# Optimization experiments

Hardware: AMD Instinct MI355X
Metric: run time of the kernel (lower is better)

## Reference

```python
import jax, jax.numpy as jnp
import numpy as np

N, E = 30000, 600000
D_NODE, E_DIM, H1, H2, D_OUT = 128, 128, 256, 128, 128


def setup_inputs() -> dict:
    key = jax.random.key(0)
    ks = jax.random.split(key, 24)
    w = lambda k, shape: jax.random.normal(k, shape, jnp.float32) * 0.05
    return {
        "node_feat": jax.random.normal(ks[0], (N, D_NODE), jnp.float32),
        "src": jax.random.randint(ks[1], (E,), 0, N, jnp.int32),
        "dst": jax.random.randint(ks[2], (E,), 0, N, jnp.int32),
        "W_e1": w(ks[3], (2 * D_NODE + E_DIM, H1)), "b_e1": w(ks[4], (H1,)),
        "W_e2": w(ks[5], (H1, E_DIM)), "b_e2": w(ks[6], (E_DIM,)),
        "W_n1": w(ks[7], (D_NODE + E_DIM, H1)), "b_n1": w(ks[8], (H1,)),
        "W_n2": w(ks[9], (H1, H2)), "b_n2": w(ks[10], (H2,)),
        "W_el1": w(ks[11], (2 * H2, H1)), "b_el1": w(ks[12], (H1,)),
        "W_el2": w(ks[13], (H1, E_DIM)), "b_el2": w(ks[14], (E_DIM,)),
        "W_logit": w(ks[15], (E_DIM, 2)), "b_logit": w(ks[16], (2,)),
        "W_nro": w(ks[17], (H2, D_OUT)), "b_nro": w(ks[18], (D_OUT,)),
        "W_ero": w(ks[19], (E_DIM, D_OUT)), "b_ero": w(ks[20], (D_OUT,)),
        "msg_passing_steps": 2,
    }


def reference(node_feat, src, dst,
              W_e1, b_e1, W_e2, b_e2,
              W_n1, b_n1, W_n2, b_n2,
              W_el1, b_el1, W_el2, b_el2,
              W_logit, b_logit, W_nro, b_nro, W_ero, b_ero,
              msg_passing_steps):
    n_nodes = node_feat.shape[0]
    edge_dim = W_e2.shape[1]
    # incoming messages 'h', initialized to zeros
    h = jnp.zeros((n_nodes, edge_dim), node_feat.dtype)
    for _ in range(msg_passing_steps):
        # apply_edges: edge_feat = fc_edge2(relu(fc_edge([h_src, nf_src, nf_dst])))
        inp = jnp.concatenate([h[src], node_feat[src], node_feat[dst]], axis=-1)  # [E, edge_dim+2*D]
        edge_feat = jax.nn.relu(inp @ W_e1 + b_e1) @ W_e2 + b_e2                   # [E, edge_dim]
        # update_all with fn.sum: scatter-sum messages into destination nodes
        h = jax.ops.segment_sum(edge_feat, dst, num_segments=n_nodes)
    # apply_nodes: node_feat <- fc_node2(relu(fc_node([node_feat, h])))
    nf = jax.nn.relu(jnp.concatenate([node_feat, h], axis=-1) @ W_n1 + b_n1) @ W_n2 + b_n2  # [N, H2]
    n_out = nf @ W_nro + b_nro
    # compute_edge_logits: symmetric edge MLP over updated node reps
    s, d = nf[src], nf[dst]
    edge_mlp = lambda x: jax.nn.relu(x @ W_el1 + b_el1) @ W_el2 + b_el2
    comb = edge_mlp(jnp.concatenate([s, d], axis=-1)) + edge_mlp(jnp.concatenate([d, s], axis=-1))
    e_out_readout = comb @ W_ero + b_ero
    e_out = comb @ W_logit + b_logit
    return n_out, e_out_readout, e_out
```

## Files before the change

kernel.cpp:

```cpp
#include <hip/hip_runtime.h>
#include <hip/hip_bf16.h>

typedef __bf16 bf16;
typedef unsigned short u16;
typedef bf16 bf16x8 __attribute__((ext_vector_type(8)));
typedef bf16 bf16x4 __attribute__((ext_vector_type(4)));
typedef float f32x4 __attribute__((ext_vector_type(4)));

constexpr int NN = 30000;
constexpr int NE = 600000;
constexpr int D  = 128;

__device__ inline f32x4 mfma16(bf16x8 a, bf16x8 b, f32x4 c) {
    return __builtin_amdgcn_mfma_f32_16x16x32_bf16(a, b, c, 0, 0, 0);
}
__device__ inline bf16x8 ld8(const bf16* p) {
    return *reinterpret_cast<const bf16x8*>(p);
}
__device__ inline bf16x8 cvt8(const float* p) {
    float4 v0 = reinterpret_cast<const float4*>(p)[0];
    float4 v1 = reinterpret_cast<const float4*>(p)[1];
    bf16x8 r;
    r[0] = (bf16)v0.x; r[1] = (bf16)v0.y; r[2] = (bf16)v0.z; r[3] = (bf16)v0.w;
    r[4] = (bf16)v1.x; r[5] = (bf16)v1.y; r[6] = (bf16)v1.z; r[7] = (bf16)v1.w;
    return r;
}
__device__ inline int swz512(int row, int byteInRow) {
    return row * 512 + (byteInRow ^ ((row & 15) << 4));
}

struct TMat { const float* src; bf16* dst; int K; int Nc; };
struct TPack { TMat m[12]; };

__global__ void transpose_cast_kernel(TPack p) {
    TMat mm = p.m[blockIdx.x];
    int total = mm.K * mm.Nc;
    for (int idx = blockIdx.y * blockDim.x + threadIdx.x; idx < total;
         idx += gridDim.y * blockDim.x) {
        int c = idx / mm.K;
        int k = idx - c * mm.K;
        mm.dst[idx] = (bf16)mm.src[k * mm.Nc + c];
    }
}

__global__ void fuse_kernel(const float* __restrict__ W_el2,
                            const float* __restrict__ W_ero,
                            const float* __restrict__ W_logit,
                            const float* __restrict__ b_el2,
                            const float* __restrict__ b_ero,
                            const float* __restrict__ b_logit,
                            bf16* __restrict__ W2eroT, bf16* __restrict__ W2lgT,
                            float* __restrict__ b2ero, float* __restrict__ b2lg) {
    int k = blockIdx.x;
    int c = threadIdx.x;
    if (c >= 144) return;
    if (k < 256) {
        if (c < 128) {
            float s = 0.f;
            for (int j = 0; j < 128; ++j) s += W_el2[k * 128 + j] * W_ero[j * 128 + c];
            W2eroT[c * 256 + k] = (bf16)s;
        } else {
            int cc = c - 128;
            float s = 0.f;
            if (cc < 2) for (int j = 0; j < 128; ++j) s += W_el2[k * 128 + j] * W_logit[j * 2 + cc];
            W2lgT[cc * 256 + k] = (bf16)s;
        }
    } else {
        if (c < 128) {
            float s = b_ero[c];
            for (int j = 0; j < 128; ++j) s += 2.f * b_el2[j] * W_ero[j * 128 + c];
            b2ero[c] = s;
        } else if (c < 130) {
            int cc = c - 128;
            float s = b_logit[cc];
            for (int j = 0; j < 128; ++j) s += 2.f * b_el2[j] * W_logit[j * 2 + cc];
            b2lg[cc] = s;
        }
    }
}

__global__ void fuse2_kernel(const float* __restrict__ W_e2,
                             const float* __restrict__ W_e1,
                             const float* __restrict__ W_n1,
                             const float* __restrict__ b_e2,
                             bf16* __restrict__ WcsT, bf16* __restrict__ WcnT,
                             float* __restrict__ bcs, float* __restrict__ bcn) {
    int k = blockIdx.x;
    int c = threadIdx.x;
    if (k < 256) {
        float s1 = 0.f, s2 = 0.f;
        for (int j = 0; j < 128; ++j) {
            float w = W_e2[k * 128 + j];
            s1 += w * W_e1[j * 256 + c];
            s2 += w * W_n1[(128 + j) * 256 + c];
        }
        WcsT[c * 256 + k] = (bf16)s1;
        WcnT[c * 256 + k] = (bf16)s2;
    } else {
        float s1 = 0.f, s2 = 0.f;
        for (int j = 0; j < 128; ++j) {
            float b = b_e2[j];
            s1 += b * W_e1[j * 256 + c];
            s2 += b * W_n1[(128 + j) * 256 + c];
        }
        bcs[c] = s1;
        bcn[c] = s2;
    }
}

__global__ void hist_kernel(const int* __restrict__ dst, int* __restrict__ counts) {
    int e = blockIdx.x * blockDim.x + threadIdx.x;
    if (e < NE) atomicAdd(counts + dst[e], 1);
}

__global__ void scan_kernel(const int* __restrict__ counts, int* __restrict__ offsets,
                            int* __restrict__ cursor) {
    __shared__ int part[1024];
    const int t = threadIdx.x;
    const int base = t * 30;
    int local[30];
    int s = 0;
#pragma unroll
    for (int i = 0; i < 30; ++i) {
        int idx = base + i;
        int v = (idx < NN) ? counts[idx] : 0;
        local[i] = s;
        s += v;
    }
    part[t] = s;
    __syncthreads();
    for (int off = 1; off < 1024; off <<= 1) {
        int x = (t >= off) ? part[t - off] : 0;
        __syncthreads();
        part[t] += x;
        __syncthreads();
    }
    int chunkExcl = (t == 0) ? 0 : part[t - 1];
#pragma unroll
    for (int i = 0; i < 30; ++i) {
        int idx = base + i;
        if (idx < NN) {
            int excl = chunkExcl + local[i];
            offsets[idx] = excl;
            cursor[idx] = excl;
        }
    }
    if (t == 0) offsets[NN] = NE;
}

__global__ void scatter_kernel(const int* __restrict__ src, const int* __restrict__ dst,
                               int* __restrict__ cursor, int* __restrict__ perm,
                               u16* __restrict__ srcS, u16* __restrict__ dstS) {
    int e = blockIdx.x * blockDim.x + threadIdx.x;
    if (e < NE) {
        int d = dst[e];
        int p = atomicAdd(cursor + d, 1);
        perm[p] = e;
        srcS[p] = (u16)src[e];
        dstS[p] = (u16)d;
    }
}

template<bool IN_BF16>
__global__ void __launch_bounds__(256, 4)
node_pre_kernel(const float* __restrict__ inF, const bf16* __restrict__ inB,
                const bf16* __restrict__ WT,
                const float* __restrict__ bias0,
                bf16* __restrict__ O1, bf16* __restrict__ O2) {
    const int half = blockIdx.y;
    const int r0 = blockIdx.x * 64;
    const int t = threadIdx.x, wv = t >> 6, l = t & 63, lr = l & 15, qk = l >> 4;
    int row[4];
#pragma unroll
    for (int m = 0; m < 4; ++m) { int r = r0 + m * 16 + lr; row[m] = r < NN ? r : NN - 1; }
    int coln[4];
#pragma unroll
    for (int n = 0; n < 4; ++n) coln[n] = wv * 64 + n * 16 + lr;
    f32x4 acc[4][4];
#pragma unroll
    for (int m = 0; m < 4; ++m)
#pragma unroll
        for (int n = 0; n < 4; ++n) acc[m][n] = 0.f;
#pragma unroll
    for (int ks = 0; ks < 4; ++ks) {
        const int kg = ks * 32 + qk * 8;
        bf16x8 a[4], b[4];
#pragma unroll
        for (int m = 0; m < 4; ++m)
            a[m] = IN_BF16 ? ld8(inB + row[m] * D + kg) : cvt8(inF + row[m] * D + kg);
#pragma unroll
        for (int n = 0; n < 4; ++n) b[n] = ld8(WT + (half * 256 + coln[n]) * 128 + kg);
#pragma unroll
        for (int m = 0; m < 4; ++m)
#pragma unroll
            for (int n = 0; n < 4; ++n) acc[m][n] = mfma16(a[m], b[n], acc[m][n]);
    }
    bf16* O = half ? O2 : O1;
#pragma unroll
    for (int n = 0; n < 4; ++n) {
        float bia = (half == 0 && bias0) ? bias0[coln[n]] : 0.f;
#pragma unroll
        for (int m = 0; m < 4; ++m)
#pragma unroll
            for (int j = 0; j < 4; ++j) {
                int gr = r0 + m * 16 + qk * 4 + j;
                if (gr < NN) O[gr * 256 + coln[n]] = (bf16)(acc[m][n][j] + bia);
            }
    }
}

__global__ void __launch_bounds__(256, 4)
s2_fused_kernel(const bf16* __restrict__ T, const bf16* __restrict__ WcsT,
                const float* __restrict__ bcs, const int* __restrict__ deg,
                bf16* __restrict__ S) {
    const int r0 = blockIdx.x * 64;
    const int t = threadIdx.x, wv = t >> 6, l = t & 63, lr = l & 15, qk = l >> 4;
    int row[4];
#pragma unroll
    for (int m = 0; m < 4; ++m) { int r = r0 + m * 16 + lr; row[m] = r < NN ? r : NN - 1; }
    int coln[4];
#pragma unroll
    for (int n = 0; n < 4; ++n) coln[n] = wv * 64 + n * 16 + lr;
    f32x4 acc[4][4];
#pragma unroll
    for (int m = 0; m < 4; ++m)
#pragma unroll
        for (int n = 0; n < 4; ++n) acc[m][n] = 0.f;
#pragma unroll
    for (int ks = 0; ks < 8; ++ks) {
        const int kg = ks * 32 + qk * 8;
        bf16x8 a[4], b[4];
#pragma unroll
        for (int m = 0; m < 4; ++m) a[m] = ld8(T + (size_t)row[m] * 256 + kg);
#pragma unroll
        for (int n = 0; n < 4; ++n) b[n] = ld8(WcsT + coln[n] * 256 + kg);
#pragma unroll
        for (int m = 0; m < 4; ++m)
#pragma unroll
            for (int n = 0; n < 4; ++n) acc[m][n] = mfma16(a[m], b[n], acc[m][n]);
    }
#pragma unroll
    for (int n = 0; n < 4; ++n) {
        float bw = bcs[coln[n]];
#pragma unroll
        for (int m = 0; m < 4; ++m)
#pragma unroll
            for (int j = 0; j < 4; ++j) {
                int gr = r0 + m * 16 + qk * 4 + j;
                if (gr < NN) {
                    int idx = gr * 256 + coln[n];
                    S[idx] = (bf16)((float)S[idx] + acc[m][n][j] + (float)deg[gr] * bw);
                }
            }
    }
}

__global__ void __launch_bounds__(256, 4)
s2_update_kernel(const float* __restrict__ h1, const bf16* __restrict__ WtopT,
                 bf16* __restrict__ S) {
    const int r0 = blockIdx.x * 64;
    const int t = threadIdx.x, wv = t >> 6, l = t & 63, lr = l & 15, qk = l >> 4;
    int row[4];
#pragma unroll
    for (int m = 0; m < 4; ++m) { int r = r0 + m * 16 + lr; row[m] = r < NN ? r : NN - 1; }
    int coln[4];
#pragma unroll
    for (int n = 0; n < 4; ++n) coln[n] = wv * 64 + n * 16 + lr;
    f32x4 acc[4][4];
#pragma unroll
    for (int m = 0; m < 4; ++m)
#pragma unroll
        for (int n = 0; n < 4; ++n) acc[m][n] = 0.f;
#pragma unroll
    for (int ks = 0; ks < 4; ++ks) {
        const int kg = ks * 32 + qk * 8;
        bf16x8 a[4], b[4];
#pragma unroll
        for (int m = 0; m < 4; ++m) a[m] = cvt8(h1 + (size_t)row[m] * D + kg);
#pragma unroll
        for (int n = 0; n < 4; ++n) b[n] = ld8(WtopT + coln[n] * 128 + kg);
#pragma unroll
        for (int m = 0; m < 4; ++m)
#pragma unroll
            for (int n = 0; n < 4; ++n) acc[m][n] = mfma16(a[m], b[n], acc[m][n]);
    }
#pragma unroll
    for (int n = 0; n < 4; ++n)
#pragma unroll
        for (int m = 0; m < 4; ++m)
#pragma unroll
            for (int j = 0; j < 4; ++j) {
                int gr = r0 + m * 16 + qk * 4 + j;
                if (gr < NN) {
                    int idx = gr * 256 + coln[n];
                    S[idx] = (bf16)((float)S[idx] + acc[m][n][j]);
                }
            }
}

__global__ void __launch_bounds__(256, 8)
seg_sum_kernel(const bf16* __restrict__ S, const bf16* __restrict__ Bm,
               const int* __restrict__ offsets, const u16* __restrict__ srcS,
               bf16* __restrict__ T) {
    const int gw = (blockIdx.x * blockDim.x + threadIdx.x) >> 6;
    if (gw >= NN) return;
    const int l = threadIdx.x & 63;
    const int beg = offsets[gw], end = offsets[gw + 1];
    bf16x4 bv = *reinterpret_cast<const bf16x4*>(Bm + (size_t)gw * 256 + l * 4);
    const float b0 = (float)bv[0], b1 = (float)bv[1], b2 = (float)bv[2], b3 = (float)bv[3];
    float t0 = 0.f, t1 = 0.f, t2 = 0.f, t3 = 0.f;
    int i = beg;
    for (; i + 4 <= end; i += 4) {
        int s0 = srcS[i], s1 = srcS[i + 1], s2 = srcS[i + 2], s3 = srcS[i + 3];
        bf16x4 a0 = *reinterpret_cast<const bf16x4*>(S + (size_t)s0 * 256 + l * 4);
        bf16x4 a1 = *reinterpret_cast<const bf16x4*>(S + (size_t)s1 * 256 + l * 4);
        bf16x4 a2 = *reinterpret_cast<const bf16x4*>(S + (size_t)s2 * 256 + l * 4);
        bf16x4 a3 = *reinterpret_cast<const bf16x4*>(S + (size_t)s3 * 256 + l * 4);
        float v;
        v = (float)a0[0] + b0; t0 += v > 0.f ? v : 0.f;
        v = (float)a0[1] + b1; t1 += v > 0.f ? v : 0.f;
        v = (float)a0[2] + b2; t2 += v > 0.f ? v : 0.f;
        v = (float)a0[3] + b3; t3 += v > 0.f ? v : 0.f;
        v = (float)a1[0] + b0; t0 += v > 0.f ? v : 0.f;
        v = (float)a1[1] + b1; t1 += v > 0.f ? v : 0.f;
        v = (float)a1[2] + b2; t2 += v > 0.f ? v : 0.f;
        v = (float)a1[3] + b3; t3 += v > 0.f ? v : 0.f;
        v = (float)a2[0] + b0; t0 += v > 0.f ? v : 0.f;
        v = (float)a2[1] + b1; t1 += v > 0.f ? v : 0.f;
        v = (float)a2[2] + b2; t2 += v > 0.f ? v : 0.f;
        v = (float)a2[3] + b3; t3 += v > 0.f ? v : 0.f;
        v = (float)a3[0] + b0; t0 += v > 0.f ? v : 0.f;
        v = (float)a3[1] + b1; t1 += v > 0.f ? v : 0.f;
        v = (float)a3[2] + b2; t2 += v > 0.f ? v : 0.f;
        v = (float)a3[3] + b3; t3 += v > 0.f ? v : 0.f;
    }
    for (; i < end; ++i) {
        int s0 = srcS[i];
        bf16x4 a0 = *reinterpret_cast<const bf16x4*>(S + (size_t)s0 * 256 + l * 4);
        float v;
        v = (float)a0[0] + b0; t0 += v > 0.f ? v : 0.f;
        v = (float)a0[1] + b1; t1 += v > 0.f ? v : 0.f;
        v = (float)a0[2] + b2; t2 += v > 0.f ? v : 0.f;
        v = (float)a0[3] + b3; t3 += v > 0.f ? v : 0.f;
    }
    bf16x4 o;
    o[0] = (bf16)t0; o[1] = (bf16)t1; o[2] = (bf16)t2; o[3] = (bf16)t3;
    *reinterpret_cast<bf16x4*>(T + (size_t)gw * 256 + l * 4) = o;
}

__global__ void __launch_bounds__(256, 2)
node_mlp_fused(const float* __restrict__ node_feat,
               const bf16* __restrict__ T2,
               const bf16* __restrict__ Wn1T,
               const bf16* __restrict__ WcnT,
               const bf16* __restrict__ Wn2T,
               const float* __restrict__ b_n1,
               const float* __restrict__ bcn,
               const int* __restrict__ deg,
               const float* __restrict__ b_n2,
               bf16* __restrict__ nf2_bf) {
    __shared__ __align__(16) char sH[64 * 512];
    const int t = threadIdx.x, wv = t >> 6, l = t & 63, lr = l & 15, qk = l >> 4;
    const int r0 = blockIdx.x * 64;
    int row[4];
#pragma unroll
    for (int m = 0; m < 4; ++m) { int r = r0 + m * 16 + lr; row[m] = r < NN ? r : NN - 1; }
    int coln[4];
#pragma unroll
    for (int n = 0; n < 4; ++n) coln[n] = wv * 64 + n * 16 + lr;
    f32x4 acc[4][4];
#pragma unroll
    for (int m = 0; m < 4; ++m)
#pragma unroll
        for (int n = 0; n < 4; ++n) acc[m][n] = 0.f;
#pragma unroll
    for (int ks = 0; ks < 4; ++ks) {
        const int kg = ks * 32 + qk * 8;
        bf16x8 a[4], b[4];
#pragma unroll
        for (int m = 0; m < 4; ++m) a[m] = cvt8(node_feat + (size_t)row[m] * D + kg);
#pragma unroll
        for (int n = 0; n < 4; ++n) b[n] = ld8(Wn1T + coln[n] * 256 + kg);
#pragma unroll
        for (int m = 0; m < 4; ++m)
#pragma unroll
            for (int n = 0; n < 4; ++n) acc[m][n] = mfma16(a[m], b[n], acc[m][n]);
    }
#pragma unroll
    for (int ks = 0; ks < 8; ++ks) {
        const int kg = ks * 32 + qk * 8;
        bf16x8 a[4], b[4];
#pragma unroll
        for (int m = 0; m < 4; ++m) a[m] = ld8(T2 + (size_t)row[m] * 256 + kg);
#pragma unroll
        for (int n = 0; n < 4; ++n) b[n] = ld8(WcnT + coln[n] * 256 + kg);
#pragma unroll
        for (int m = 0; m < 4; ++m)
#pragma unroll
            for (int n = 0; n < 4; ++n) acc[m][n] = mfma16(a[m], b[n], acc[m][n]);
    }
#pragma unroll
    for (int n = 0; n < 4; ++n) {
        float bia = b_n1[coln[n]];
        float bw  = bcn[coln[n]];
#pragma unroll
        for (int m = 0; m < 4; ++m)
#pragma unroll
            for (int j = 0; j < 4; ++j) {
                int r = m * 16 + qk * 4 + j;
                int gr = r0 + r;
                float dg = (gr < NN) ? (float)deg[gr] : 0.f;
                float v = acc[m][n][j] + bia + dg * bw;
                v = v > 0.f ? v : 0.f;
                *reinterpret_cast<bf16*>(sH + swz512(r, coln[n] * 2)) = (bf16)v;
            }
    }
    __syncthreads();
    int col2[2];
#pragma unroll
    for (int n = 0; n < 2; ++n) col2[n] = wv * 32 + n * 16 + lr;
    f32x4 acc2[4][2];
#pragma unroll
    for (int m = 0; m < 4; ++m)
#pragma unroll
        for (int n = 0; n < 2; ++n) acc2[m][n] = 0.f;
#pragma unroll
    for (int ks = 0; ks < 8; ++ks) {
        const int k0 = ks * 32 + qk * 8;
        bf16x8 a[4], b[2];
#pragma unroll
        for (int m = 0; m < 4; ++m)
            a[m] = *reinterpret_cast<const bf16x8*>(sH + swz512(m * 16 + lr, k0 * 2));
#pragma unroll
        for (int n = 0; n < 2; ++n) b[n] = ld8(Wn2T + col2[n] * 256 + k0);
#pragma unroll
        for (int m = 0; m < 4; ++m)
#pragma unroll
            for (int n = 0; n < 2; ++n) acc2[m][n] = mfma16(a[m], b[n], acc2[m][n]);
    }
#pragma unroll
    for (int n = 0; n < 2; ++n) {
        float bia = b_n2[col2[n]];
#pragma unroll
        for (int m = 0; m < 4; ++m)
#pragma unroll
            for (int j = 0; j < 4; ++j) {
                int gr = r0 + m * 16 + qk * 4 + j;
                if (gr < NN) nf2_bf[(size_t)gr * D + col2[n]] = (bf16)(acc2[m][n][j] + bia);
            }
    }
}

__global__ void __launch_bounds__(256, 2)
node_mlp_kernel(const float* __restrict__ node_feat,
                const float* __restrict__ h2,
                const bf16* __restrict__ Wn1T,
                const bf16* __restrict__ Wn2T,
                const float* __restrict__ b_n1,
                const float* __restrict__ b_n2,
                bf16* __restrict__ nf2_bf) {
    __shared__ __align__(16) char sH[64 * 512];
    const int t = threadIdx.x, wv = t >> 6, l = t & 63, lr = l & 15, qk = l >> 4;
    const int r0 = blockIdx.x * 64;
    int row[4];
#pragma unroll
    for (int m = 0; m < 4; ++m) { int r = r0 + m * 16 + lr; row[m] = r < NN ? r : NN - 1; }
    int coln[4];
#pragma unroll
    for (int n = 0; n < 4; ++n) coln[n] = wv * 64 + n * 16 + lr;
    f32x4 acc[4][4];
#pragma unroll
    for (int m = 0; m < 4; ++m)
#pragma unroll
        for (int n = 0; n < 4; ++n) acc[m][n] = 0.f;
#pragma unroll
    for (int ks = 0; ks < 4; ++ks) {
        const int kg = ks * 32 + qk * 8;
        bf16x8 a[4], b[4];
#pragma unroll
        for (int m = 0; m < 4; ++m) a[m] = cvt8(node_feat + (size_t)row[m] * D + kg);
#pragma unroll
        for (int n = 0; n < 4; ++n) b[n] = ld8(Wn1T + coln[n] * 256 + kg);
#pragma unroll
        for (int m = 0; m < 4; ++m)
#pragma unroll
            for (int n = 0; n < 4; ++n) acc[m][n] = mfma16(a[m], b[n], acc[m][n]);
#pragma unroll
        for (int m = 0; m < 4; ++m) a[m] = cvt8(h2 + (size_t)row[m] * D + kg);
#pragma unroll
        for (int n = 0; n < 4; ++n) b[n] = ld8(Wn1T + coln[n] * 256 + 128 + kg);
#pragma unroll
        for (int m = 0; m < 4; ++m)
#pragma unroll
            for (int n = 0; n < 4; ++n) acc[m][n] = mfma16(a[m], b[n], acc[m][n]);
    }
#pragma unroll
    for (int n = 0; n < 4; ++n) {
        float bia = b_n1[coln[n]];
#pragma unroll
        for (int m = 0; m < 4; ++m)
#pragma unroll
            for (int j = 0; j < 4; ++j) {
                int r = m * 16 + qk * 4 + j;
                float v = acc[m][n][j] + bia;
                v = v > 0.f ? v : 0.f;
                *reinterpret_cast<bf16*>(sH + swz512(r, coln[n] * 2)) = (bf16)v;
            }
    }
    __syncthreads();
    int col2[2];
#pragma unroll
    for (int n = 0; n < 2; ++n) col2[n] = wv * 32 + n * 16 + lr;
    f32x4 acc2[4][2];
#pragma unroll
    for (int m = 0; m < 4; ++m)
#pragma unroll
        for (int n = 0; n < 2; ++n) acc2[m][n] = 0.f;
#pragma unroll
    for (int ks = 0; ks < 8; ++ks) {
        const int k0 = ks * 32 + qk * 8;
        bf16x8 a[4], b[2];
#pragma unroll
        for (int m = 0; m < 4; ++m)
            a[m] = *reinterpret_cast<const bf16x8*>(sH + swz512(m * 16 + lr, k0 * 2));
#pragma unroll
        for (int n = 0; n < 2; ++n) b[n] = ld8(Wn2T + col2[n] * 256 + k0);
#pragma unroll
        for (int m = 0; m < 4; ++m)
#pragma unroll
            for (int n = 0; n < 2; ++n) acc2[m][n] = mfma16(a[m], b[n], acc2[m][n]);
    }
#pragma unroll
    for (int n = 0; n < 2; ++n) {
        float bia = b_n2[col2[n]];
#pragma unroll
        for (int m = 0; m < 4; ++m)
#pragma unroll
            for (int j = 0; j < 4; ++j) {
                int gr = r0 + m * 16 + qk * 4 + j;
                if (gr < NN) nf2_bf[(size_t)gr * D + col2[n]] = (bf16)(acc2[m][n][j] + bia);
            }
    }
}

__global__ void __launch_bounds__(256, 4)
h_gemm_kernel(const bf16* __restrict__ T, const bf16* __restrict__ We2T,
              const float* __restrict__ b_e2, const int* __restrict__ deg,
              bf16* __restrict__ h) {
    const int r0 = blockIdx.x * 64;
    const int t = threadIdx.x, wv = t >> 6, l = t & 63, lr = l & 15, qk = l >> 4;
    int row[4];
#pragma unroll
    for (int m = 0; m < 4; ++m) { int r = r0 + m * 16 + lr; row[m] = r < NN ? r : NN - 1; }
    int col2[2];
#pragma unroll
    for (int n = 0; n < 2; ++n) col2[n] = wv * 32 + n * 16 + lr;
    f32x4 acc[4][2];
#pragma unroll
    for (int m = 0; m < 4; ++m)
#pragma unroll
        for (int n = 0; n < 2; ++n) acc[m][n] = 0.f;
#pragma unroll
    for (int ks = 0; ks < 8; ++ks) {
        const int kg = ks * 32 + qk * 8;
        bf16x8 a[4], b[2];
#pragma unroll
        for (int m = 0; m < 4; ++m) a[m] = ld8(T + (size_t)row[m] * 256 + kg);
#pragma unroll
        for (int n = 0; n < 2; ++n) b[n] = ld8(We2T + col2[n] * 256 + kg);
#pragma unroll
        for (int m = 0; m < 4; ++m)
#pragma unroll
            for (int n = 0; n < 2; ++n) acc[m][n] = mfma16(a[m], b[n], acc[m][n]);
    }
#pragma unroll
    for (int n = 0; n < 2; ++n) {
        float bw = b_e2[col2[n]];
#pragma unroll
        for (int m = 0; m < 4; ++m)
#pragma unroll
            for (int j = 0; j < 4; ++j) {
                int gr = r0 + m * 16 + qk * 4 + j;
                if (gr < NN)
                    h[(size_t)gr * D + col2[n]] = (bf16)(acc[m][n][j] + (float)deg[gr] * bw);
            }
    }
}

__global__ void __launch_bounds__(256, 4)
edge_logit_sorted(const bf16* __restrict__ U, const bf16* __restrict__ V,
                  const int* __restrict__ perm, const u16* __restrict__ srcS,
                  const u16* __restrict__ dstS,
                  const bf16* __restrict__ W2eroT, const bf16* __restrict__ W2lgT,
                  const float* __restrict__ b2ero, const float* __restrict__ b2lg,
                  float* __restrict__ e_ro, float* __restrict__ e_lg) {
    __shared__ int s_e[128];
    __shared__ int s_s[128];
    __shared__ int s_d[128];
    const int t = threadIdx.x, wv = t >> 6, l = t & 63, lr = l & 15, qk = l >> 4;
    const int bid = (int)blockIdx.x;
    const int cpx = (int)(gridDim.x >> 3);
    const int sbid = (bid & 7) * cpx + (bid >> 3);
    const int p0 = sbid * 128;
    if (t < 128) {
        int p = min(p0 + t, NE - 1);
        s_e[t] = perm[p];
        s_s[t] = (int)srcS[p];
        s_d[t] = (int)dstS[p];
    }
    __syncthreads();

    int is[2], id[2];
#pragma unroll
    for (int m = 0; m < 2; ++m) {
        int el = wv * 32 + m * 16 + lr;
        is[m] = s_s[el];
        id[m] = s_d[el];
    }
    f32x4 aro[2][8];
    f32x4 alg[2];
#pragma unroll
    for (int m = 0; m < 2; ++m) {
        alg[m] = 0.f;
#pragma unroll
        for (int n = 0; n < 8; ++n) aro[m][n] = 0.f;
    }
#pragma unroll
    for (int ks = 0; ks < 8; ++ks) {
        const int kg = ks * 32 + qk * 8;
        bf16x8 a[2];
#pragma unroll
        for (int m = 0; m < 2; ++m) {
            bf16x8 us = ld8(U + (size_t)is[m] * 256 + kg);
            bf16x8 vd = ld8(V + (size_t)id[m] * 256 + kg);
            bf16x8 ud = ld8(U + (size_t)id[m] * 256 + kg);
            bf16x8 vs = ld8(V + (size_t)is[m] * 256 + kg);
#pragma unroll
            for (int i = 0; i < 8; ++i) {
                float f1 = (float)us[i] + (float)vd[i]; f1 = f1 > 0.f ? f1 : 0.f;
                float f2 = (float)ud[i] + (float)vs[i]; f2 = f2 > 0.f ? f2 : 0.f;
                a[m][i] = (bf16)(f1 + f2);
            }
        }
#pragma unroll
        for (int n = 0; n < 8; ++n) {
            bf16x8 b = ld8(W2eroT + (n * 16 + lr) * 256 + kg);
#pragma unroll
            for (int m = 0; m < 2; ++m) aro[m][n] = mfma16(a[m], b, aro[m][n]);
        }
        bf16x8 blg = ld8(W2lgT + lr * 256 + kg);
#pragma unroll
        for (int m = 0; m < 2; ++m) alg[m] = mfma16(a[m], blg, alg[m]);
    }
#pragma unroll
    for (int n = 0; n < 8; ++n) {
        int col = n * 16 + lr;
        float bia = b2ero[col];
#pragma unroll
        for (int m = 0; m < 2; ++m)
#pragma unroll
            for (int j = 0; j < 4; ++j) {
                int el = wv * 32 + m * 16 + qk * 4 + j;
                __builtin_nontemporal_store(aro[m][n][j] + bia,
                                            e_ro + (size_t)s_e[el] * D + col);
            }
    }
    if (lr < 2) {
        float bia = b2lg[lr];
#pragma unroll
        for (int m = 0; m < 2; ++m)
#pragma unroll
            for (int j = 0; j < 4; ++j) {
                int el = wv * 32 + m * 16 + qk * 4 + j;
                e_lg[(size_t)s_e[el] * 2 + lr] = alg[m][j] + bia;
            }
    }
}

__global__ void __launch_bounds__(256, 4)
edge_msg_kernel(const bf16* __restrict__ S, const bf16* __restrict__ Bm,
                const int* __restrict__ src, const int* __restrict__ dst,
                const bf16* __restrict__ We2T,
                const float* __restrict__ b_e2,
                float* __restrict__ h_out) {
    __shared__ int s_src[128];
    __shared__ int s_dst[128];
    const int t = threadIdx.x, wv = t >> 6, l = t & 63, lr = l & 15, qk = l >> 4;
    const int e0 = blockIdx.x * 128;
    if (t < 128)      s_src[t] = src[min(e0 + t, NE - 1)];
    else              s_dst[t - 128] = dst[min(e0 + t - 128, NE - 1)];
    __syncthreads();
    const bf16* pS[2];
    const bf16* pB[2];
#pragma unroll
    for (int m = 0; m < 2; ++m) {
        int el = wv * 32 + m * 16 + lr;
        pS[m] = S + s_src[el] * 256;
        pB[m] = Bm + s_dst[el] * 256;
    }
    f32x4 acc[2][8];
#pragma unroll
    for (int m = 0; m < 2; ++m)
#pragma unroll
        for (int n = 0; n < 8; ++n) acc[m][n] = 0.f;
#pragma unroll
    for (int ks = 0; ks < 8; ++ks) {
        const int kg = ks * 32 + qk * 8;
        bf16x8 a[2];
#pragma unroll
        for (int m = 0; m < 2; ++m) {
            bf16x8 sa = ld8(pS[m] + kg);
            bf16x8 sb = ld8(pB[m] + kg);
#pragma unroll
            for (int i = 0; i < 8; ++i) {
                float f = (float)sa[i] + (float)sb[i];
                a[m][i] = (bf16)(f > 0.f ? f : 0.f);
            }
        }
#pragma unroll
        for (int n = 0; n < 8; ++n) {
            bf16x8 b = ld8(We2T + (n * 16 + lr) * 256 + kg);
#pragma unroll
            for (int m = 0; m < 2; ++m) acc[m][n] = mfma16(a[m], b, acc[m][n]);
        }
    }
#pragma unroll
    for (int n = 0; n < 8; ++n) {
        int col = n * 16 + lr;
        float bia = b_e2[col];
#pragma unroll
        for (int m = 0; m < 2; ++m)
#pragma unroll
            for (int j = 0; j < 4; ++j) {
                int el = wv * 32 + m * 16 + qk * 4 + j;
                if (e0 + el < NE)
                    atomicAdd(h_out + s_dst[el] * D + col, acc[m][n][j] + bia);
            }
    }
}

__global__ void __launch_bounds__(256, 4)
edge_logit_fast(const bf16* __restrict__ U, const bf16* __restrict__ V,
                const int* __restrict__ src, const int* __restrict__ dst,
                const bf16* __restrict__ W2eroT,
                const bf16* __restrict__ W2lgT,
                const float* __restrict__ b2ero, const float* __restrict__ b2lg,
                float* __restrict__ e_ro, float* __restrict__ e_lg) {
    __shared__ int s_src[128];
    __shared__ int s_dst[128];
    const int t = threadIdx.x, wv = t >> 6, l = t & 63, lr = l & 15, qk = l >> 4;
    const int e0 = blockIdx.x * 128;
    if (t < 128)      s_src[t] = src[min(e0 + t, NE - 1)];
    else              s_dst[t - 128] = dst[min(e0 + t - 128, NE - 1)];
    __syncthreads();
    int is[2], id[2];
#pragma unroll
    for (int m = 0; m < 2; ++m) {
        int el = wv * 32 + m * 16 + lr;
        is[m] = s_src[el];
        id[m] = s_dst[el];
    }
    f32x4 aro[2][8];
    f32x4 alg[2];
#pragma unroll
    for (int m = 0; m < 2; ++m) {
        alg[m] = 0.f;
#pragma unroll
        for (int n = 0; n < 8; ++n) aro[m][n] = 0.f;
    }
#pragma unroll
    for (int ks = 0; ks < 8; ++ks) {
        const int kg = ks * 32 + qk * 8;
        bf16x8 a[2];
#pragma unroll
        for (int m = 0; m < 2; ++m) {
            bf16x8 us = ld8(U + is[m] * 256 + kg);
            bf16x8 vd = ld8(V + id[m] * 256 + kg);
            bf16x8 ud = ld8(U + id[m] * 256 + kg);
            bf16x8 vs = ld8(V + is[m] * 256 + kg);
#pragma unroll
            for (int i = 0; i < 8; ++i) {
                float f1 = (float)us[i] + (float)vd[i]; f1 = f1 > 0.f ? f1 : 0.f;
                float f2 = (float)ud[i] + (float)vs[i]; f2 = f2 > 0.f ? f2 : 0.f;
                a[m][i] = (bf16)(f1 + f2);
            }
        }
#pragma unroll
        for (int n = 0; n < 8; ++n) {
            bf16x8 b = ld8(W2eroT + (n * 16 + lr) * 256 + kg);
#pragma unroll
            for (int m = 0; m < 2; ++m) aro[m][n] = mfma16(a[m], b, aro[m][n]);
        }
        bf16x8 blg = ld8(W2lgT + lr * 256 + kg);
#pragma unroll
        for (int m = 0; m < 2; ++m) alg[m] = mfma16(a[m], blg, alg[m]);
    }
#pragma unroll
    for (int n = 0; n < 8; ++n) {
        int col = n * 16 + lr;
        float bia = b2ero[col];
#pragma unroll
        for (int m = 0; m < 2; ++m)
#pragma unroll
            for (int j = 0; j < 4; ++j) {
                int el = wv * 32 + m * 16 + qk * 4 + j;
                int e = e0 + el;
                if (e < NE) e_ro[e * D + col] = aro[m][n][j] + bia;
            }
    }
    if (lr < 2) {
        float bia = b2lg[lr];
#pragma unroll
        for (int m = 0; m < 2; ++m)
#pragma unroll
            for (int j = 0; j < 4; ++j) {
                int el = wv * 32 + m * 16 + qk * 4 + j;
                int e = e0 + el;
                if (e < NE) e_lg[e * 2 + lr] = alg[m][j] + bia;
            }
    }
}

__global__ void __launch_bounds__(256, 4)
nro_kernel(const bf16* __restrict__ nf2_bf, const bf16* __restrict__ WnroT,
           const float* __restrict__ b_nro, float* __restrict__ n_out) {
    const int r0 = blockIdx.x * 64;
    const int t = threadIdx.x, wv = t >> 6, l = t & 63, lr = l & 15, qk = l >> 4;
    int row[4];
#pragma unroll
    for (int m = 0; m < 4; ++m) { int r = r0 + m * 16 + lr; row[m] = r < NN ? r : NN - 1; }
    int col2[2];
#pragma unroll
    for (int n = 0; n < 2; ++n) col2[n] = wv * 32 + n * 16 + lr;
    f32x4 acc[4][2];
#pragma unroll
    for (int m = 0; m < 4; ++m)
#pragma unroll
        for (int n = 0; n < 2; ++n) acc[m][n] = 0.f;
#pragma unroll
    for (int ks = 0; ks < 4; ++ks) {
        const int kg = ks * 32 + qk * 8;
        bf16x8 a[4], b[2];
#pragma unroll
        for (int m = 0; m < 4; ++m) a[m] = ld8(nf2_bf + (size_t)row[m] * D + kg);
#pragma unroll
        for (int n = 0; n < 2; ++n) b[n] = ld8(WnroT + col2[n] * 128 + kg);
#pragma unroll
        for (int m = 0; m < 4; ++m)
#pragma unroll
            for (int n = 0; n < 2; ++n) acc[m][n] = mfma16(a[m], b[n], acc[m][n]);
    }
#pragma unroll
    for (int n = 0; n < 2; ++n) {
        float bia = b_nro[col2[n]];
#pragma unroll
        for (int m = 0; m < 4; ++m)
#pragma unroll
            for (int j = 0; j < 4; ++j) {
                int gr = r0 + m * 16 + qk * 4 + j;
                if (gr < NN) n_out[(size_t)gr * D + col2[n]] = acc[m][n][j] + bia;
            }
    }
}

extern "C" void kernel_launch(void* const* d_in, const int* in_sizes, int n_in,
                              void* d_out, int out_size, void* d_ws, size_t ws_size,
                              hipStream_t stream) {
    const float* node_feat = (const float*)d_in[0];
    const int*   src   = (const int*)d_in[1];
    const int*   dst   = (const int*)d_in[2];
    const float* W_e1  = (const float*)d_in[3];
    const float* b_e1  = (const float*)d_in[4];
    const float* W_e2  = (const float*)d_in[5];
    const float* b_e2  = (const float*)d_in[6];
    const float* W_n1  = (const float*)d_in[7];
    const float* b_n1  = (const float*)d_in[8];
    const float* W_n2  = (const float*)d_in[9];
    const float* b_n2  = (const float*)d_in[10];
    const float* W_el1 = (const float*)d_in[11];
    const float* b_el1 = (const float*)d_in[12];
    const float* W_el2 = (const float*)d_in[13];
    const float* b_el2 = (const float*)d_in[14];
    const float* W_logit = (const float*)d_in[15];
    const float* b_logit = (const float*)d_in[16];
    const float* W_nro = (const float*)d_in[17];
    const float* b_nro = (const float*)d_in[18];
    const float* W_ero = (const float*)d_in[19];
    const float* b_ero = (const float*)d_in[20];

    char* ws = (char*)d_ws;
    bf16* wb = (bf16*)ws;
    bf16* WmbT   = wb;
    bf16* WtopT  = wb + 65536;
    bf16* We2T   = wb + 98304;
    bf16* Wn1T   = wb + 131072;
    bf16* Wn2T   = wb + 196608;
    bf16* WuvT   = wb + 229376;
    bf16* WnroT  = wb + 294912;
    bf16* W2eroT = wb + 311296;
    bf16* W2lgT  = wb + 344064;
    bf16* WcsT   = wb + 348160;
    bf16* WcnT   = wb + 413696;
    float* fb    = (float*)(ws + 960000);
    float* b2ero = fb;
    float* b2lg  = fb + 128;
    float* bcs   = fb + 256;
    float* bcn   = fb + 512;

    float* out   = (float*)d_out;
    float* n_out = out;
    float* e_ro  = out + 3840000;
    float* e_lg  = out + 80640000;

    TPack pk;
    pk.m[0]  = {W_e1 + 128 * 256, WmbT,              128, 256};
    pk.m[1]  = {W_e1 + 256 * 256, WmbT + 256 * 128,  128, 256};
    pk.m[2]  = {W_e1,             WtopT,             128, 256};
    pk.m[3]  = {W_e2,             We2T,              256, 128};
    pk.m[4]  = {W_n1,             Wn1T,              256, 256};
    pk.m[5]  = {W_n2,             Wn2T,              256, 128};
    pk.m[6]  = {W_el1,            WuvT,              128, 256};
    pk.m[7]  = {W_el1 + 128 * 256, WuvT + 256 * 128, 128, 256};
    pk.m[8]  = {W_nro,            WnroT,             128, 128};
    pk.m[9]  = {W_nro,            WnroT,             128, 128};
    pk.m[10] = {W_nro,            WnroT,             128, 128};
    pk.m[11] = {W_nro,            WnroT,             128, 128};

    const size_t NEED_NEW = 28888576;

    if (ws_size >= NEED_NEW) {
        char* eb = (char*)e_ro;
        bf16* S    = (bf16*)(eb);
        bf16* Bm   = (bf16*)(eb + 15360000);
        bf16* T    = (bf16*)(eb + 30720000);
        int* counts  = (int*)(eb + 61440000);
        int* offsets = (int*)(eb + 61560000);
        int* cursor  = (int*)(eb + 61680004);
        bf16* U    = (bf16*)n_out;
        bf16* nf2_bf = (bf16*)(ws + 1048576);
        bf16* Vbuf   = (bf16*)(ws + 8728576);
        int*  perm   = (int*)(ws + 24088576);
        u16*  srcS   = (u16*)(ws + 26488576);
        u16*  dstS   = (u16*)(ws + 27688576);

        transpose_cast_kernel<<<dim3(12, 40), 256, 0, stream>>>(pk);
        fuse_kernel<<<257, 160, 0, stream>>>(W_el2, W_ero, W_logit, b_el2, b_ero, b_logit,
                                             W2eroT, W2lgT, b2ero, b2lg);
        fuse2_kernel<<<257, 256, 0, stream>>>(W_e2, W_e1, W_n1, b_e2,
                                              WcsT, WcnT, bcs, bcn);
        hipMemsetAsync(counts, 0, NN * 4, stream);
        hist_kernel<<<(NE + 255) / 256, 256, 0, stream>>>(dst, counts);
        scan_kernel<<<1, 1024, 0, stream>>>(counts, offsets, cursor);
        scatter_kernel<<<(NE + 255) / 256, 256, 0, stream>>>(src, dst, cursor,
                                                             perm, srcS, dstS);
        node_pre_kernel<false><<<dim3(469, 2), 256, 0, stream>>>(
            node_feat, nullptr, WmbT, b_e1, S, Bm);
        seg_sum_kernel<<<7500, 256, 0, stream>>>(S, Bm, offsets, srcS, T);
        s2_fused_kernel<<<469, 256, 0, stream>>>(T, WcsT, bcs, counts, S);
        seg_sum_kernel<<<7500, 256, 0, stream>>>(S, Bm, offsets, srcS, T);
        node_mlp_fused<<<469, 256, 0, stream>>>(
            node_feat, T, Wn1T, WcnT, Wn2T, b_n1, bcn, counts, b_n2, nf2_bf);
        node_pre_kernel<true><<<dim3(469, 2), 256, 0, stream>>>(
            nullptr, nf2_bf, WuvT, b_el1, U, Vbuf);
        edge_logit_sorted<<<4688, 256, 0, stream>>>(
            U, Vbuf, perm, srcS, dstS, W2eroT, W2lgT, b2ero, b2lg, e_ro, e_lg);
        nro_kernel<<<469, 256, 0, stream>>>(nf2_bf, WnroT, b_nro, n_out);
    } else {
        bf16* nf2_bf = (bf16*)(ws + 1048576);
        bf16* Vbuf   = (bf16*)(ws + 9000000);
        float* h1f = n_out;
        bf16*  S   = (bf16*)e_ro;
        bf16*  Bm  = (bf16*)((char*)e_ro + 15360000);
        float* h2f = (float*)((char*)e_ro + 30720000);
        bf16*  U   = (bf16*)n_out;

        transpose_cast_kernel<<<dim3(12, 40), 256, 0, stream>>>(pk);
        fuse_kernel<<<257, 160, 0, stream>>>(W_el2, W_ero, W_logit, b_el2, b_ero, b_logit,
                                             W2eroT, W2lgT, b2ero, b2lg);
        hipMemsetAsync(h1f, 0, (size_t)NN * D * 4, stream);
        hipMemsetAsync(h2f, 0, (size_t)NN * D * 4, stream);
        node_pre_kernel<false><<<dim3(469, 2), 256, 0, stream>>>(
            node_feat, nullptr, WmbT, b_e1, S, Bm);
        edge_msg_kernel<<<4688, 256, 0, stream>>>(S, Bm, src, dst, We2T, b_e2, h1f);
        s2_update_kernel<<<469, 256, 0, stream>>>(h1f, WtopT, S);
        edge_msg_kernel<<<4688, 256, 0, stream>>>(S, Bm, src, dst, We2T, b_e2, h2f);
        node_mlp_kernel<<<469, 256, 0, stream>>>(
            node_feat, h2f, Wn1T, Wn2T, b_n1, b_n2, nf2_bf);
        node_pre_kernel<true><<<dim3(469, 2), 256, 0, stream>>>(
            nullptr, nf2_bf, WuvT, b_el1, U, Vbuf);
        edge_logit_fast<<<4688, 256, 0, stream>>>(
            U, Vbuf, src, dst, W2eroT, W2lgT, b2ero, b2lg, e_ro, e_lg);
        nro_kernel<<<469, 256, 0, stream>>>(nf2_bf, WnroT, b_nro, n_out);
    }
}
```

Baseline: 735.7 us.

## Sort edge-logit edges by source-bucket then destination for gather locality

Adds a second counting sort whose key is (src>>12, dst), so the edge-logit kernel processes edges grouped by coarse source range and then by destination. The aim is better cache locality on the U/V gathers. The first sort now only produces srcS for the segment sums, and the kernel reads dst through perm2. It adds a histogram, a single-block scan over 240K keys and a scatter pass, and it switches the e_ro stores from nontemporal to regular stores.

```diff
diff --git a/kernel.cpp b/kernel.cpp
--- a/kernel.cpp
+++ b/kernel.cpp
@@ -10,6 +10,7 @@
 constexpr int NN = 30000;
 constexpr int NE = 600000;
 constexpr int D  = 128;
+constexpr int NKEY = 8 * NN;
 
 __device__ inline f32x4 mfma16(bf16x8 a, bf16x8 b, f32x4 c) {
     return __builtin_amdgcn_mfma_f32_16x16x32_bf16(a, b, c, 0, 0, 0);
@@ -149,15 +150,61 @@
 }
 
 __global__ void scatter_kernel(const int* __restrict__ src, const int* __restrict__ dst,
-                               int* __restrict__ cursor, int* __restrict__ perm,
-                               u16* __restrict__ srcS, u16* __restrict__ dstS) {
+                               int* __restrict__ cursor, u16* __restrict__ srcS) {
     int e = blockIdx.x * blockDim.x + threadIdx.x;
     if (e < NE) {
         int d = dst[e];
         int p = atomicAdd(cursor + d, 1);
-        perm[p] = e;
         srcS[p] = (u16)src[e];
-        dstS[p] = (u16)d;
+    }
+}
+
+__global__ void hist2_kernel(const int* __restrict__ src, const int* __restrict__ dst,
+                             int* __restrict__ counts2) {
+    int e = blockIdx.x * blockDim.x + threadIdx.x;
+    if (e < NE) {
+        int k = (src[e] >> 12) * NN + dst[e];
+        atomicAdd(counts2 + k, 1);
+    }
+}
+
+__global__ void scan2_kernel(const int* __restrict__ counts2, int* __restrict__ cursor2) {
+    __shared__ int part[1024];
+    const int t = threadIdx.x;
+    const int base = t * 235;
+    int s = 0;
+    for (int i = 0; i < 235; ++i) {
+        int idx = base + i;
+        if (idx < NKEY) s += counts2[idx];
+    }
+    part[t] = s;
+    __syncthreads();
+    for (int off = 1; off < 1024; off <<= 1) {
+        int x = (t >= off) ? part[t - off] : 0;
+        __syncthreads();
+        part[t] += x;
+        __syncthreads();
+    }
+    int run = (t == 0) ? 0 : part[t - 1];
+    for (int i = 0; i < 235; ++i) {
+        int idx = base + i;
+        if (idx < NKEY) {
+            cursor2[idx] = run;
+            run += counts2[idx];
+        }
+    }
+}
+
+__global__ void scatter2_kernel(const int* __restrict__ src, const int* __restrict__ dst,
+                                int* __restrict__ cursor2, int* __restrict__ perm2,
+                                u16* __restrict__ srcS2) {
+    int e = blockIdx.x * blockDim.x + threadIdx.x;
+    if (e < NE) {
+        int s = src[e];
+        int k = (s >> 12) * NN + dst[e];
+        int p = atomicAdd(cursor2 + k, 1);
+        perm2[p] = e;
+        srcS2[p] = (u16)s;
     }
 }
 
@@ -589,8 +636,8 @@
 
 __global__ void __launch_bounds__(256, 4)
 edge_logit_sorted(const bf16* __restrict__ U, const bf16* __restrict__ V,
-                  const int* __restrict__ perm, const u16* __restrict__ srcS,
-                  const u16* __restrict__ dstS,
+                  const int* __restrict__ perm2, const u16* __restrict__ srcS2,
+                  const int* __restrict__ dst,
                   const bf16* __restrict__ W2eroT, const bf16* __restrict__ W2lgT,
                   const float* __restrict__ b2ero, const float* __restrict__ b2lg,
                   float* __restrict__ e_ro, float* __restrict__ e_lg) {
@@ -604,9 +651,10 @@
     const int p0 = sbid * 128;
     if (t < 128) {
         int p = min(p0 + t, NE - 1);
-        s_e[t] = perm[p];
-        s_s[t] = (int)srcS[p];
-        s_d[t] = (int)dstS[p];
+        int e = perm2[p];
+        s_e[t] = e;
+        s_s[t] = (int)srcS2[p];
+        s_d[t] = dst[e];
     }
     __syncthreads();
 
@@ -661,8 +709,7 @@
 #pragma unroll
             for (int j = 0; j < 4; ++j) {
                 int el = wv * 32 + m * 16 + qk * 4 + j;
-                __builtin_nontemporal_store(aro[m][n][j] + bia,
-                                            e_ro + (size_t)s_e[el] * D + col);
+                e_ro[(size_t)s_e[el] * D + col] = aro[m][n][j] + bia;
             }
     }
     if (lr < 2) {
@@ -936,12 +983,14 @@
         int* counts  = (int*)(eb + 61440000);
         int* offsets = (int*)(eb + 61560000);
         int* cursor  = (int*)(eb + 61680004);
+        int* counts2 = (int*)(eb + 61800004);
+        int* cursor2 = (int*)(eb + 62760004);
         bf16* U    = (bf16*)n_out;
         bf16* nf2_bf = (bf16*)(ws + 1048576);
         bf16* Vbuf   = (bf16*)(ws + 8728576);
-        int*  perm   = (int*)(ws + 24088576);
-        u16*  srcS   = (u16*)(ws + 26488576);
-        u16*  dstS   = (u16*)(ws + 27688576);
+        u16*  srcS   = (u16*)(ws + 24088576);
+        int*  perm2  = (int*)(ws + 25288576);
+        u16*  srcS2  = (u16*)(ws + 27688576);
 
         transpose_cast_kernel<<<dim3(12, 40), 256, 0, stream>>>(pk);
         fuse_kernel<<<257, 160, 0, stream>>>(W_el2, W_ero, W_logit, b_el2, b_ero, b_logit,
@@ -949,10 +998,14 @@
         fuse2_kernel<<<257, 256, 0, stream>>>(W_e2, W_e1, W_n1, b_e2,
                                               WcsT, WcnT, bcs, bcn);
         hipMemsetAsync(counts, 0, NN * 4, stream);
+        hipMemsetAsync(counts2, 0, NKEY * 4, stream);
         hist_kernel<<<(NE + 255) / 256, 256, 0, stream>>>(dst, counts);
+        hist2_kernel<<<(NE + 255) / 256, 256, 0, stream>>>(src, dst, counts2);
         scan_kernel<<<1, 1024, 0, stream>>>(counts, offsets, cursor);
-        scatter_kernel<<<(NE + 255) / 256, 256, 0, stream>>>(src, dst, cursor,
-                                                             perm, srcS, dstS);
+        scan2_kernel<<<1, 1024, 0, stream>>>(counts2, cursor2);
+        scatter_kernel<<<(NE + 255) / 256, 256, 0, stream>>>(src, dst, cursor, srcS);
+        scatter2_kernel<<<(NE + 255) / 256, 256, 0, stream>>>(src, dst, cursor2,
+                                                              perm2, srcS2);
         node_pre_kernel<false><<<dim3(469, 2), 256, 0, stream>>>(
             node_feat, nullptr, WmbT, b_e1, S, Bm);
         seg_sum_kernel<<<7500, 256, 0, stream>>>(S, Bm, offsets, srcS, T);
@@ -963,7 +1016,7 @@
         node_pre_kernel<true><<<dim3(469, 2), 256, 0, stream>>>(
             nullptr, nf2_bf, WuvT, b_el1, U, Vbuf);
         edge_logit_sorted<<<4688, 256, 0, stream>>>(
-            U, Vbuf, perm, srcS, dstS, W2eroT, W2lgT, b2ero, b2lg, e_ro, e_lg);
+            U, Vbuf, perm2, srcS2, dst, W2eroT, W2lgT, b2ero, b2lg, e_ro, e_lg);
         nro_kernel<<<469, 256, 0, stream>>>(nf2_bf, WnroT, b_nro, n_out);
     } else {
         bf16* nf2_bf = (bf16*)(ws + 1048576);
```

After: 1.311 ms. 78.2% more time.
